# Kernel optimization log

Measured on AMD Instinct MI355X. Metric: run time of the kernel, lower is better.

Reference implementation:

```python
import jax, jax.numpy as jnp
import numpy as np

N = 500_000
E = 5_000_000
DIM = 16
LR = 0.005
THRESHOLD = 0.0


def setup_inputs() -> dict:
    key = jax.random.key(0)
    ks = jax.random.split(key, 8)
    s = 1.0 / np.sqrt(DIM)
    return {
        "x": jax.random.normal(ks[0], (N, DIM), jnp.float32),
        "edge_index": jax.random.randint(ks[1], (2, E), 0, N, dtype=jnp.int32),
        "W1": jax.random.normal(ks[2], (DIM, DIM), jnp.float32) * s,
        "b1": jnp.zeros((DIM,), jnp.float32),
        "W2": jax.random.normal(ks[3], (DIM, DIM), jnp.float32) * s,
        "b2": jnp.zeros((DIM,), jnp.float32),
        "W3": jax.random.normal(ks[4], (DIM, DIM), jnp.float32) * s,
        "b3": jnp.zeros((DIM,), jnp.float32),
        "positive": 0,  # negative sample -> nonzero loss branch
    }


def gcn_conv(x, edge_index, W, b):
    # PyG GCNConv: h = x @ W.T, add self-loops, symmetric norm, aggregate at dst.
    n = x.shape[0]
    loop = jnp.arange(n, dtype=edge_index.dtype)
    src = jnp.concatenate([edge_index[0], loop])
    dst = jnp.concatenate([edge_index[1], loop])
    deg = jax.ops.segment_sum(jnp.ones_like(dst, x.dtype), dst, num_segments=n)
    dinv = jnp.where(deg > 0, jax.lax.rsqrt(deg), 0.0)
    norm = dinv[src] * dinv[dst]  # [E+N]
    h = x @ W.T  # [N, out]
    msg = norm[:, None] * h[src]  # irregular gather, memory-bound
    return jax.ops.segment_sum(msg, dst, num_segments=n) + b


def local_loss(g, positive):
    t = THRESHOLD
    if positive:
        return jnp.where(g > t + 10.0, 0.0,
               jnp.where(g < t - 10.0, t - g, jnp.log1p(jnp.exp(t - g))))
    return jnp.where(g > t + 10.0, t + g,
           jnp.where(g < t - 10.0, 0.0, jnp.log1p(jnp.exp(g + t))))


def reference(x, edge_index, W1, b1, W2, b2, W3, b3, positive):
    # Note: the original computes activation_normalizer(x) and loss_derivative(g)
    # into z/driv_loss but immediately overwrites both -> dead code, omitted.
    agg = jnp.float32(0.0)
    Wc, bc = W1, b1  # conv1 params, updated in-place each layer in the original
    x_cur = x
    for (W, b) in ((W1, b1), (W2, b2), (W3, b3)):
        z = jax.nn.relu(gcn_conv(x_cur, edge_index, W, b))
        goodness = jnp.sum(z * z) / z.shape[1]
        agg = agg + local_loss(goodness, positive)
        d = 2.0 * jnp.abs(z)            # activation_gradient(z)
        wd = d * d                      # weighted_deriv
        dW = x_cur.T @ wd               # [in, out]
        db = jnp.sum(wd, axis=0)
        Wc = Wc - LR * dW.T
        bc = bc - LR * db
        x_cur = z
    return agg, Wc, bc
```

## Files before the change

kernel.cpp:

```cpp
#include <hip/hip_runtime.h>
#include <math.h>

#define TPB 256
#define TPB_P 512
#define TPB_A 512
#define LRATE 0.005f

#define LOG_NPB 10
#define NPB (1 << LOG_NPB)
#define CAP 14336

#define LOG_SUP 13
#define NS1 64
#define CAP1 90112
#define NS2 8
#define CHUNK 4096
#define CPT (CHUNK / TPB_P)
#define R1 4
#define R2 8
#define RS 4

#define NTILE 64

#define FXS  65536.0f
#define FXSI (1.0f / 65536.0f)
#define FXBIAS (1 << 20)

#if __has_builtin(__builtin_amdgcn_cvt_f32_fp8) && __has_builtin(__builtin_amdgcn_cvt_pk_fp8_f32)
__device__ __forceinline__ float fp8_dec(unsigned char v) {
    return __builtin_amdgcn_cvt_f32_fp8((int)v, 0);
}
__device__ __forceinline__ unsigned fp8_pk4(float a, float b, float c, float d) {
    int w = __builtin_amdgcn_cvt_pk_fp8_f32(a, b, 0, false);
    w = __builtin_amdgcn_cvt_pk_fp8_f32(c, d, w, true);
    return (unsigned)w;
}
#else
__device__ __forceinline__ unsigned char fp8_enc1(float f) {
    unsigned u = __float_as_uint(f);
    unsigned s = (u >> 24) & 0x80u;
    u &= 0x7FFFFFFFu;
    if (u >= 0x43E00000u) return (unsigned char)(s | 0x7E);
    if (u < 0x3C800000u) {
        float a = __uint_as_float(u);
        int m = (int)rintf(a * 512.f);
        return (unsigned char)(s | (unsigned)m);
    }
    unsigned mant = u & 0x7FFFFFu;
    unsigned rest = mant & 0xFFFFFu;
    unsigned keep = u >> 20;
    keep += (rest > 0x80000u || (rest == 0x80000u && (keep & 1u))) ? 1u : 0u;
    int eb = (int)(keep >> 3) - 127 + 7;
    return (unsigned char)(s | (unsigned)((eb << 3) | (int)(keep & 7u)));
}
__device__ __forceinline__ float fp8_dec(unsigned char v) {
    unsigned s = ((unsigned)(v & 0x80u)) << 24;
    unsigned e = (v >> 3) & 0xFu;
    unsigned m = v & 7u;
    if (e == 0) {
        float r = (float)m * 0.001953125f;
        return (v & 0x80u) ? -r : r;
    }
    return __uint_as_float(s | ((e + 120u) << 23) | (m << 20));
}
__device__ __forceinline__ unsigned fp8_pk4(float a, float b, float c, float d) {
    return (unsigned)fp8_enc1(a) | ((unsigned)fp8_enc1(b) << 8) |
           ((unsigned)fp8_enc1(c) << 16) | ((unsigned)fp8_enc1(d) << 24);
}
#endif

#if __has_builtin(__builtin_amdgcn_cvt_pk_f32_fp8)
typedef float __attribute__((ext_vector_type(2))) f32x2;
__device__ __forceinline__ void fp8_dec4(unsigned w, float& a, float& b, float& c, float& d) {
    f32x2 lo = __builtin_amdgcn_cvt_pk_f32_fp8((int)w, false);
    f32x2 hi = __builtin_amdgcn_cvt_pk_f32_fp8((int)w, true);
    a = lo[0]; b = lo[1]; c = hi[0]; d = hi[1];
}
#else
__device__ __forceinline__ void fp8_dec4(unsigned w, float& a, float& b, float& c, float& d) {
    a = fp8_dec((unsigned char)(w & 0xFFu));
    b = fp8_dec((unsigned char)((w >> 8) & 0xFFu));
    c = fp8_dec((unsigned char)((w >> 16) & 0xFFu));
    d = fp8_dec((unsigned char)((w >> 24) & 0xFFu));
}
#endif

__device__ __forceinline__ unsigned long long pack2(float f0, float f1) {
    unsigned lo = (unsigned)(FXBIAS + (int)(f0 * FXS));
    unsigned hi = (unsigned)(FXBIAS + (int)(f1 * FXS));
    return (unsigned long long)lo | ((unsigned long long)hi << 32);
}

__global__ __launch_bounds__(TPB_P) void k_part1(const int* __restrict__ src,
                                                 const int* __restrict__ dst,
                                                 int* __restrict__ bcur1,
                                                 int* __restrict__ grec1,
                                                 int E) {
    __shared__ int hist[R1][NS1];
    __shared__ int lcur[R1][NS1];
    __shared__ int lstart[NS1], tot[NS1], gbase[NS1];
    __shared__ int lbuf[CHUNK];
    __shared__ unsigned char bbuf[CHUNK];
    int t = threadIdx.x;
    int g = t & (R1 - 1);
    int chunkBase = blockIdx.x * CHUNK;
    for (int i = t; i < R1 * NS1; i += TPB_P) (&hist[0][0])[i] = 0;
    __syncthreads();

    int myb[CPT], myrec[CPT];
#pragma unroll
    for (int k = 0; k < CPT; k++) {
        int e = chunkBase + k * TPB_P + t;
        if (e < E) {
            int d = dst[e];
            int s = src[e];
            myb[k] = d >> LOG_SUP;
            myrec[k] = (s << LOG_SUP) | (d & ((1 << LOG_SUP) - 1));
            atomicAdd(&hist[g][myb[k]], 1);
        } else myb[k] = -1;
    }
    __syncthreads();
    if (t < NS1) {
        int s = 0;
#pragma unroll
        for (int r = 0; r < R1; r++) s += hist[r][t];
        tot[t] = s;
    }
    __syncthreads();
    if (t == 0) {
        int run = 0;
        for (int b = 0; b < NS1; b++) { lstart[b] = run; run += tot[b]; }
    }
    __syncthreads();
    if (t < NS1) {
        int run = lstart[t];
#pragma unroll
        for (int r = 0; r < R1; r++) { lcur[r][t] = run; run += hist[r][t]; }
        if (tot[t] > 0) gbase[t] = atomicAdd(&bcur1[t * 16], tot[t]);
    }
    __syncthreads();
#pragma unroll
    for (int k = 0; k < CPT; k++) {
        if (myb[k] >= 0) {
            int p = atomicAdd(&lcur[g][myb[k]], 1);
            lbuf[p] = myrec[k];
            bbuf[p] = (unsigned char)myb[k];
        }
    }
    __syncthreads();
    int total = E - chunkBase; if (total > CHUNK) total = CHUNK;
    for (int p = t; p < total; p += TPB_P) {
        int b = (int)bbuf[p];
        int pos = gbase[b] + (p - lstart[b]);
        if (pos < CAP1) grec1[(size_t)b * CAP1 + pos] = lbuf[p];
    }
}

__global__ __launch_bounds__(TPB_P) void k_part2(const int* __restrict__ bcur1,
                                                 const int* __restrict__ grec1,
                                                 int* __restrict__ bcur,
                                                 int* __restrict__ grecU) {
    __shared__ int hist[R2][NS2];
    __shared__ int lcur[R2][NS2];
    __shared__ int lstart[NS2], tot[NS2], gbase[NS2];
    __shared__ int lbuf[CHUNK];
    __shared__ unsigned char bbuf[CHUNK];
    int t = threadIdx.x;
    int g = t & (R2 - 1);
    int s = blockIdx.x;
    int cnt1 = bcur1[s * 16]; if (cnt1 > CAP1) cnt1 = CAP1;
    int chunkBase = blockIdx.y * CHUNK;
    if (chunkBase >= cnt1) return;
    int total = cnt1 - chunkBase; if (total > CHUNK) total = CHUNK;
    for (int i = t; i < R2 * NS2; i += TPB_P) (&hist[0][0])[i] = 0;
    __syncthreads();

    int myb[CPT], myrec[CPT];
#pragma unroll
    for (int k = 0; k < CPT; k++) {
        int i = chunkBase + k * TPB_P + t;
        if (i < cnt1) {
            int r = grec1[(size_t)s * CAP1 + i];
            int sub = (r >> LOG_NPB) & (NS2 - 1);
            myb[k] = sub;
            myrec[k] = (int)((((unsigned)r) >> LOG_SUP) << LOG_NPB) | (r & (NPB - 1));
            atomicAdd(&hist[g][sub], 1);
        } else myb[k] = -1;
    }
    __syncthreads();
    if (t < NS2) {
        int c = 0;
#pragma unroll
        for (int r = 0; r < R2; r++) c += hist[r][t];
        tot[t] = c;
    }
    __syncthreads();
    if (t == 0) {
        int run = 0;
        for (int b = 0; b < NS2; b++) { lstart[b] = run; run += tot[b]; }
    }
    __syncthreads();
    if (t < NS2) {
        int run = lstart[t];
#pragma unroll
        for (int r = 0; r < R2; r++) { lcur[r][t] = run; run += hist[r][t]; }
        if (tot[t] > 0) gbase[t] = atomicAdd(&bcur[(s * NS2 + t) * 16], tot[t]);
    }
    __syncthreads();
#pragma unroll
    for (int k = 0; k < CPT; k++) {
        if (myb[k] >= 0) {
            int p = atomicAdd(&lcur[g][myb[k]], 1);
            lbuf[p] = myrec[k];
            bbuf[p] = (unsigned char)myb[k];
        }
    }
    __syncthreads();
    for (int p = t; p < total; p += TPB_P) {
        int b = (int)bbuf[p];
        int pos = gbase[b] + (p - lstart[b]);
        if (pos < CAP) grecU[(size_t)(s * NS2 + b) * CAP + pos] = lbuf[p];
    }
}

__global__ __launch_bounds__(TPB_P) void k_sort(const int* __restrict__ bcur,
                                                const int* __restrict__ grecU,
                                                int* __restrict__ grec,
                                                float* __restrict__ dinv, int N) {
    __shared__ int lbuf[CAP];
    __shared__ int deg[NPB];
    __shared__ int hist[RS][NTILE];
    __shared__ int curp[RS][NTILE];
    __shared__ int lstart[NTILE], tot[NTILE];
    int t = threadIdx.x;
    int g = t & (RS - 1);
    int b = blockIdx.x;
    int cnt = bcur[b * 16]; if (cnt > CAP) cnt = CAP;
    const size_t base = (size_t)b * CAP;

    for (int i = t; i < RS * NTILE; i += TPB_P) (&hist[0][0])[i] = 0;
    for (int i = t; i < NPB; i += TPB_P) deg[i] = 0;
    __syncthreads();
    for (int i = t; i < cnt; i += TPB_P) {
        int r = grecU[base + i];
        lbuf[i] = r;
        atomicAdd(&deg[r & (NPB - 1)], 1);
        atomicAdd(&hist[g][((unsigned)r) >> 23], 1);
    }
    __syncthreads();
    if (t < NTILE) {
        int c = 0;
#pragma unroll
        for (int r = 0; r < RS; r++) c += hist[r][t];
        tot[t] = c;
    }
    __syncthreads();
    if (t == 0) {
        int run = 0;
#pragma unroll
        for (int k = 0; k < NTILE; k++) { lstart[k] = run; run += tot[k]; }
    }
    __syncthreads();
    if (t < NTILE) {
        int run = lstart[t];
#pragma unroll
        for (int r = 0; r < RS; r++) { curp[r][t] = run; run += hist[r][t]; }
    }
    __syncthreads();
    for (int i = t; i < cnt; i += TPB_P) {
        int r = lbuf[i];
        int p = atomicAdd(&curp[g][((unsigned)r) >> 23], 1);
        grec[base + p] = r;
    }
    int nodeBase = b << LOG_NPB;
    for (int i = t; i < NPB; i += TPB_P) {
        int node = nodeBase + i;
        if (node < N) dinv[node] = rsqrtf((float)(deg[i] + 1));
    }
}

__global__ __launch_bounds__(TPB) void k_h(const float* __restrict__ xc,
                                           const float* __restrict__ W,
                                           const float* __restrict__ dinv,
                                           unsigned* __restrict__ hp, int n) {
    __shared__ float sW[256];
    if (threadIdx.x < 256) sW[threadIdx.x] = W[threadIdx.x];
    __syncthreads();
    int i = blockIdx.x * blockDim.x + threadIdx.x;
    int stride = gridDim.x * blockDim.x;
    for (; i < n; i += stride) {
        float x[16];
        const float4* xr = (const float4*)(xc + (size_t)i * 16);
#pragma unroll
        for (int q = 0; q < 4; q++) {
            float4 v = xr[q];
            x[4*q+0] = v.x; x[4*q+1] = v.y; x[4*q+2] = v.z; x[4*q+3] = v.w;
        }
        float di = dinv[i];
        float hv[16];
#pragma unroll
        for (int j = 0; j < 16; j++) {
            float s = 0.f;
#pragma unroll
            for (int k = 0; k < 16; k++) s = fmaf(x[k], sW[j*16 + k], s);
            hv[j] = di * s;
        }
        uint4 w;
        w.x = fp8_pk4(hv[0],  hv[1],  hv[2],  hv[3]);
        w.y = fp8_pk4(hv[4],  hv[5],  hv[6],  hv[7]);
        w.z = fp8_pk4(hv[8],  hv[9],  hv[10], hv[11]);
        w.w = fp8_pk4(hv[12], hv[13], hv[14], hv[15]);
        ((uint4*)hp)[i] = w;
    }
}

__global__ __launch_bounds__(TPB_A, 4) void k_agg(const int* __restrict__ bcur,
                                                  const int* __restrict__ grec,
                                                  const float* __restrict__ dinv,
                                                  const unsigned* __restrict__ hp32,
                                                  const float* __restrict__ b,
                                                  const float* __restrict__ xc,
                                                  float* __restrict__ z,
                                                  float* __restrict__ partial,
                                                  int nb, int N) {
    __shared__ unsigned long long accP[8 * NPB];
    int t = threadIdx.x;
    int bkt = blockIdx.x;
    int cnt = bcur[bkt * 16]; if (cnt > CAP) cnt = CAP;
    const int nodeBase = bkt << LOG_NPB;
    const size_t recBase = (size_t)bkt * CAP;

    for (int i = t; i < 8 * NPB; i += TPB_A) accP[i] = 0ull;
    __syncthreads();

    int q = t & 3;
    int gi = t >> 2;
    int p0 = q * 2;
    int p1 = q * 2 + 1;
    int base = 0;
    for (; base + 512 <= cnt; base += 512) {
        int rec[4];
#pragma unroll
        for (int u = 0; u < 4; u++) rec[u] = grec[recBase + base + u * 128 + gi];
        unsigned w[4];
#pragma unroll
        for (int u = 0; u < 4; u++)
            w[u] = hp32[(size_t)(((unsigned)rec[u]) >> LOG_NPB) * 4 + q];
#pragma unroll
        for (int u = 0; u < 4; u++) {
            int dl = rec[u] & (NPB - 1);
            float f0, f1, f2, f3;
            fp8_dec4(w[u], f0, f1, f2, f3);
            atomicAdd(&accP[p0 * NPB + (dl ^ p0)], pack2(f0, f1));
            atomicAdd(&accP[p1 * NPB + (dl ^ p1)], pack2(f2, f3));
        }
    }
    for (int e = base + gi; e < cnt; e += 128) {
        int rec = grec[recBase + e];
        unsigned w = hp32[(size_t)(((unsigned)rec) >> LOG_NPB) * 4 + q];
        int dl = rec & (NPB - 1);
        float f0, f1, f2, f3;
        fp8_dec4(w, f0, f1, f2, f3);
        atomicAdd(&accP[p0 * NPB + (dl ^ p0)], pack2(f0, f1));
        atomicAdd(&accP[p1 * NPB + (dl ^ p1)], pack2(f2, f3));
    }
    __syncthreads();

    const unsigned char* hpB = (const unsigned char*)hp32;
    const int* accI32 = (const int*)accP;
    int j = t & 15;
    int g0 = t >> 4;
    int pj = j >> 1;
    int hj = j & 1;
    float bj = b[j];
    float accW[16];
#pragma unroll
    for (int k = 0; k < 16; k++) accW[k] = 0.f;
    float accB = 0.f;

    for (int i = g0; i < NPB; i += 32) {
        int node = nodeBase + i;
        if (node >= N) break;
        float di = dinv[node];
        int cdeg = (int)rintf(1.0f / (di * di)) - 1;
        int raw = accI32[(pj * NPB + (i ^ pj)) * 2 + hj];
        int ai = raw - cdeg * FXBIAS;
        float sv = fp8_dec(hpB[(size_t)node * 16 + j]);
        float aj = fmaf((float)ai, FXSI, sv);
        float zj = fmaxf(fmaf(di, aj, bj), 0.f);
        z[(size_t)node * 16 + j] = zj;
        float wdj = 4.f * zj * zj;
        accB += wdj;
        const float4* xrow = (const float4*)(xc + (size_t)node * 16);
        float4 x0 = xrow[0], x1 = xrow[1], x2 = xrow[2], x3 = xrow[3];
        accW[0]  = fmaf(x0.x, wdj, accW[0]);  accW[1]  = fmaf(x0.y, wdj, accW[1]);
        accW[2]  = fmaf(x0.z, wdj, accW[2]);  accW[3]  = fmaf(x0.w, wdj, accW[3]);
        accW[4]  = fmaf(x1.x, wdj, accW[4]);  accW[5]  = fmaf(x1.y, wdj, accW[5]);
        accW[6]  = fmaf(x1.z, wdj, accW[6]);  accW[7]  = fmaf(x1.w, wdj, accW[7]);
        accW[8]  = fmaf(x2.x, wdj, accW[8]);  accW[9]  = fmaf(x2.y, wdj, accW[9]);
        accW[10] = fmaf(x2.z, wdj, accW[10]); accW[11] = fmaf(x2.w, wdj, accW[11]);
        accW[12] = fmaf(x3.x, wdj, accW[12]); accW[13] = fmaf(x3.y, wdj, accW[13]);
        accW[14] = fmaf(x3.z, wdj, accW[14]); accW[15] = fmaf(x3.w, wdj, accW[15]);
    }
    __syncthreads();

    float (*red)[17] = (float (*)[17])accP;
#pragma unroll
    for (int k = 0; k < 16; k++) red[t][k] = accW[k];
    red[t][16] = accB;
    __syncthreads();
    if (t < 256) {
        int kk = t >> 4;
        int jj = t & 15;
        float s = 0.f;
#pragma unroll
        for (int g2 = 0; g2 < 32; g2++) s += red[g2 * 16 + jj][kk];
        partial[(size_t)(kk * 16 + jj) * nb + bkt] = s;
    }
    if (t < 16) {
        float sb = 0.f;
#pragma unroll
        for (int g2 = 0; g2 < 32; g2++) sb += red[g2 * 16 + t][16];
        partial[(size_t)(256 + t) * nb + bkt] = sb;
    }
}

__global__ __launch_bounds__(TPB) void k_reduce(const float* __restrict__ partial,
                                                float* __restrict__ acc,
                                                int nb, int total) {
    int wid = (blockIdx.x * blockDim.x + threadIdx.x) >> 6;
    int lane = threadIdx.x & 63;
    if (wid >= total) return;
    const float* p = partial + (size_t)wid * nb;
    float s = 0.f;
    for (int b = lane; b < nb; b += 64) s += p[b];
#pragma unroll
    for (int off = 32; off > 0; off >>= 1) s += __shfl_down(s, off, 64);
    if (lane == 0) acc[wid] = s;
}

__device__ __forceinline__ float local_loss_f(float g, int positive) {
    const float t = 0.0f;
    if (positive) {
        if (g > t + 10.f) return 0.f;
        if (g < t - 10.f) return t - g;
        return log1pf(expf(t - g));
    } else {
        if (g > t + 10.f) return t + g;
        if (g < t - 10.f) return 0.f;
        return log1pf(expf(g + t));
    }
}

__global__ void k_final(const float* __restrict__ W1, const float* __restrict__ b1,
                        const float* __restrict__ acc, const int* __restrict__ positive,
                        float* __restrict__ outv) {
    int t = threadIdx.x;
    if (t < 256) {
        int jj = t >> 4, kk = t & 15;
        float s = 0.f;
#pragma unroll
        for (int l = 0; l < 3; l++) s += acc[l * 272 + kk * 16 + jj];
        outv[1 + t] = W1[t] - LRATE * s;
    }
    if (t < 16) {
        float s = 0.f;
#pragma unroll
        for (int l = 0; l < 3; l++) s += acc[l * 272 + 256 + t];
        outv[257 + t] = b1[t] - LRATE * s;
    }
    if (t == 0) {
        int pos = positive[0];
        float agg = 0.f;
#pragma unroll
        for (int l = 0; l < 3; l++) {
            float g = 0.f;
#pragma unroll
            for (int jj = 0; jj < 16; jj++) g += acc[l * 272 + 256 + jj];
            g *= (1.0f / 64.0f);
            agg += local_loss_f(g, pos);
        }
        outv[0] = agg;
    }
}

extern "C" void kernel_launch(void* const* d_in, const int* in_sizes, int n_in,
                              void* d_out, int out_size, void* d_ws, size_t ws_size,
                              hipStream_t stream) {
    const float* x  = (const float*)d_in[0];
    const int*   ei = (const int*)d_in[1];
    const float* W1 = (const float*)d_in[2];
    const float* b1 = (const float*)d_in[3];
    const float* W2 = (const float*)d_in[4];
    const float* b2 = (const float*)d_in[5];
    const float* W3 = (const float*)d_in[6];
    const float* b3 = (const float*)d_in[7];
    const int* positive = (const int*)d_in[8];
    float* outv = (float*)d_out;

    const int N = in_sizes[0] / 16;
    const int E = in_sizes[1] / 2;
    const int nbuck = (N + NPB - 1) >> LOG_NPB;
    const int nsuper = (N + (1 << LOG_SUP) - 1) >> LOG_SUP;
    const int nbpad = nsuper * NS2;

    char* ws = (char*)d_ws;
    size_t off = 0;
    auto carve = [&](size_t bytes) -> void* {
        void* p = ws + off;
        off = (off + bytes + 255) & ~(size_t)255;
        return p;
    };
    int*   bcur   = (int*)  carve((size_t)(nbpad + NS1) * 16 * 4);
    int*   bcur1  = bcur + (size_t)nbpad * 16;
    int*   grec   = (int*)  carve((size_t)nbpad * CAP * 4);
    float* dinv   = (float*)carve((size_t)N * 4);
    float* acc    = (float*)carve(3 * 272 * 4);
    float* part   = (float*)carve((size_t)3 * 272 * nbuck * 4);
    unsigned* hp  = (unsigned*)carve((size_t)N * 16);
    float* P1     = (float*)carve((size_t)N * 64);
    int*   grecU  = (int*)P1;
    float* P2     = (float*)carve((size_t)N * 64);
    int*   grec1  = (int*)P2;

    hipMemsetAsync(bcur, 0, (size_t)(nbpad + NS1) * 16 * 4, stream);

    const int* src = ei;
    const int* dst = ei + E;

    int p1Blocks = (E + CHUNK - 1) / CHUNK;
    k_part1<<<p1Blocks, TPB_P, 0, stream>>>(src, dst, bcur1, grec1, E);
    dim3 g2(nsuper, CAP1 / CHUNK);
    k_part2<<<g2, TPB_P, 0, stream>>>(bcur1, grec1, bcur, grecU);
    k_sort<<<nbuck, TPB_P, 0, stream>>>(bcur, grecU, grec, dinv, N);

    const float* Ws[3] = {W1, W2, W3};
    const float* bss[3] = {b1, b2, b3};
    float* outs[3] = {P1, P2, P1};

    int nodeBlocks = (N + TPB - 1) / TPB;

    const float* xc = x;
    for (int l = 0; l < 3; l++) {
        k_h<<<nodeBlocks, TPB, 0, stream>>>(xc, Ws[l], dinv, hp, N);
        k_agg<<<nbuck, TPB_A, 0, stream>>>(bcur, grec, dinv, hp, bss[l],
                                           xc, outs[l],
                                           part + (size_t)l * 272 * nbuck, nbuck, N);
        xc = outs[l];
    }
    int totalElems = 3 * 272;
    k_reduce<<<(totalElems * 64 + TPB - 1) / TPB, TPB, 0, stream>>>(part, acc, nbuck, totalElems);
    k_final<<<1, 256, 0, stream>>>(W1, b1, acc, positive, outv);
}
```

Before: 391.4 us.

## Fuse per-layer h projection into sort and aggregation kernel epilogues

Removes the separate k_h launches. The first layer's fp8 h = dinv*(x@W1^T) is now computed at the end of k_sort. Each later layer's h is computed in the epilogue of the previous k_agg, reading the z rows that block just wrote, with the hp buffer double-buffered between layers. This saves three kernel launches and lets z be reread while it is likely still cache-resident. In exchange the aggregation kernels get longer tails with extra syncs and register pressure inside a kernel bound to 4 waves per SIMD.

After: 657.2 us. 1.68x slower.

```diff
diff --git a/kernel.cpp b/kernel.cpp
--- a/kernel.cpp
+++ b/kernel.cpp
@@ -19,7 +19,6 @@
 #define R1 4
 #define R2 8
 #define RS 4
-
 #define NTILE 64
 
 #define FXS  65536.0f
@@ -89,6 +88,31 @@
     unsigned lo = (unsigned)(FXBIAS + (int)(f0 * FXS));
     unsigned hi = (unsigned)(FXBIAS + (int)(f1 * FXS));
     return (unsigned long long)lo | ((unsigned long long)hi << 32);
+}
+
+__device__ __forceinline__ uint4 hp_row(const float* __restrict__ xrow,
+                                        const float* __restrict__ sW, float di) {
+    float xv[16];
+    const float4* xr = (const float4*)xrow;
+#pragma unroll
+    for (int q = 0; q < 4; q++) {
+        float4 v = xr[q];
+        xv[4*q+0] = v.x; xv[4*q+1] = v.y; xv[4*q+2] = v.z; xv[4*q+3] = v.w;
+    }
+    float hv[16];
+#pragma unroll
+    for (int j = 0; j < 16; j++) {
+        float s = 0.f;
+#pragma unroll
+        for (int k = 0; k < 16; k++) s = fmaf(xv[k], sW[j*16 + k], s);
+        hv[j] = di * s;
+    }
+    uint4 w;
+    w.x = fp8_pk4(hv[0],  hv[1],  hv[2],  hv[3]);
+    w.y = fp8_pk4(hv[4],  hv[5],  hv[6],  hv[7]);
+    w.z = fp8_pk4(hv[8],  hv[9],  hv[10], hv[11]);
+    w.w = fp8_pk4(hv[12], hv[13], hv[14], hv[15]);
+    return w;
 }
 
 __global__ __launch_bounds__(TPB_P) void k_part1(const int* __restrict__ src,
@@ -226,7 +250,10 @@
 __global__ __launch_bounds__(TPB_P) void k_sort(const int* __restrict__ bcur,
                                                 const int* __restrict__ grecU,
                                                 int* __restrict__ grec,
-                                                float* __restrict__ dinv, int N) {
+                                                float* __restrict__ dinv,
+                                                const float* __restrict__ x,
+                                                const float* __restrict__ W1,
+                                                unsigned* __restrict__ hp, int N) {
     __shared__ int lbuf[CAP];
     __shared__ int deg[NPB];
     __shared__ int hist[RS][NTILE];
@@ -272,45 +299,18 @@
         int p = atomicAdd(&curp[g][((unsigned)r) >> 23], 1);
         grec[base + p] = r;
     }
+    __syncthreads();
+
+    float* sW = (float*)lbuf;
+    if (t < 256) sW[t] = W1[t];
+    __syncthreads();
     int nodeBase = b << LOG_NPB;
     for (int i = t; i < NPB; i += TPB_P) {
         int node = nodeBase + i;
-        if (node < N) dinv[node] = rsqrtf((float)(deg[i] + 1));
-    }
-}
-
-__global__ __launch_bounds__(TPB) void k_h(const float* __restrict__ xc,
-                                           const float* __restrict__ W,
-                                           const float* __restrict__ dinv,
-                                           unsigned* __restrict__ hp, int n) {
-    __shared__ float sW[256];
-    if (threadIdx.x < 256) sW[threadIdx.x] = W[threadIdx.x];
-    __syncthreads();
-    int i = blockIdx.x * blockDim.x + threadIdx.x;
-    int stride = gridDim.x * blockDim.x;
-    for (; i < n; i += stride) {
-        float x[16];
-        const float4* xr = (const float4*)(xc + (size_t)i * 16);
-#pragma unroll
-        for (int q = 0; q < 4; q++) {
-            float4 v = xr[q];
-            x[4*q+0] = v.x; x[4*q+1] = v.y; x[4*q+2] = v.z; x[4*q+3] = v.w;
-        }
-        float di = dinv[i];
-        float hv[16];
-#pragma unroll
-        for (int j = 0; j < 16; j++) {
-            float s = 0.f;
-#pragma unroll
-            for (int k = 0; k < 16; k++) s = fmaf(x[k], sW[j*16 + k], s);
-            hv[j] = di * s;
-        }
-        uint4 w;
-        w.x = fp8_pk4(hv[0],  hv[1],  hv[2],  hv[3]);
-        w.y = fp8_pk4(hv[4],  hv[5],  hv[6],  hv[7]);
-        w.z = fp8_pk4(hv[8],  hv[9],  hv[10], hv[11]);
-        w.w = fp8_pk4(hv[12], hv[13], hv[14], hv[15]);
-        ((uint4*)hp)[i] = w;
+        if (node >= N) continue;
+        float di = rsqrtf((float)(deg[i] + 1));
+        dinv[node] = di;
+        ((uint4*)hp)[node] = hp_row(x + (size_t)node * 16, sW, di);
     }
 }
 
@@ -322,6 +322,8 @@
                                                   const float* __restrict__ xc,
                                                   float* __restrict__ z,
                                                   float* __restrict__ partial,
+                                                  const float* __restrict__ Wnext,
+                                                  unsigned* __restrict__ hpNext,
                                                   int nb, int N) {
     __shared__ unsigned long long accP[8 * NPB];
     int t = threadIdx.x;
@@ -423,6 +425,18 @@
         for (int g2 = 0; g2 < 32; g2++) sb += red[g2 * 16 + t][16];
         partial[(size_t)(256 + t) * nb + bkt] = sb;
     }
+
+    if (Wnext != nullptr) {
+        __syncthreads();
+        float* sW = (float*)accP;
+        if (t < 256) sW[t] = Wnext[t];
+        __syncthreads();
+        for (int i = t; i < NPB; i += TPB_A) {
+            int node = nodeBase + i;
+            if (node >= N) continue;
+            ((uint4*)hpNext)[node] = hp_row(z + (size_t)node * 16, sW, dinv[node]);
+        }
+    }
 }
 
 __global__ __launch_bounds__(TPB) void k_reduce(const float* __restrict__ partial,
@@ -517,7 +531,8 @@
     float* dinv   = (float*)carve((size_t)N * 4);
     float* acc    = (float*)carve(3 * 272 * 4);
     float* part   = (float*)carve((size_t)3 * 272 * nbuck * 4);
-    unsigned* hp  = (unsigned*)carve((size_t)N * 16);
+    unsigned* hpA = (unsigned*)carve((size_t)N * 16);
+    unsigned* hpB = (unsigned*)carve((size_t)N * 16);
     float* P1     = (float*)carve((size_t)N * 64);
     int*   grecU  = (int*)P1;
     float* P2     = (float*)carve((size_t)N * 64);
@@ -532,22 +547,18 @@
     k_part1<<<p1Blocks, TPB_P, 0, stream>>>(src, dst, bcur1, grec1, E);
     dim3 g2(nsuper, CAP1 / CHUNK);
     k_part2<<<g2, TPB_P, 0, stream>>>(bcur1, grec1, bcur, grecU);
-    k_sort<<<nbuck, TPB_P, 0, stream>>>(bcur, grecU, grec, dinv, N);
-
-    const float* Ws[3] = {W1, W2, W3};
-    const float* bss[3] = {b1, b2, b3};
-    float* outs[3] = {P1, P2, P1};
-
-    int nodeBlocks = (N + TPB - 1) / TPB;
-
-    const float* xc = x;
-    for (int l = 0; l < 3; l++) {
-        k_h<<<nodeBlocks, TPB, 0, stream>>>(xc, Ws[l], dinv, hp, N);
-        k_agg<<<nbuck, TPB_A, 0, stream>>>(bcur, grec, dinv, hp, bss[l],
-                                           xc, outs[l],
-                                           part + (size_t)l * 272 * nbuck, nbuck, N);
-        xc = outs[l];
-    }
+    k_sort<<<nbuck, TPB_P, 0, stream>>>(bcur, grecU, grec, dinv, x, W1, hpA, N);
+
+    k_agg<<<nbuck, TPB_A, 0, stream>>>(bcur, grec, dinv, hpA, b1, x,  P1,
+                                       part + (size_t)0 * 272 * nbuck,
+                                       W2, hpB, nbuck, N);
+    k_agg<<<nbuck, TPB_A, 0, stream>>>(bcur, grec, dinv, hpB, b2, P1, P2,
+                                       part + (size_t)1 * 272 * nbuck,
+                                       W3, hpA, nbuck, N);
+    k_agg<<<nbuck, TPB_A, 0, stream>>>(bcur, grec, dinv, hpA, b3, P2, P1,
+                                       part + (size_t)2 * 272 * nbuck,
+                                       nullptr, nullptr, nbuck, N);
+
     int totalElems = 3 * 272;
     k_reduce<<<(totalElems * 64 + TPB - 1) / TPB, TPB, 0, stream>>>(part, acc, nbuck, totalElems);
     k_final<<<1, 256, 0, stream>>>(W1, b1, acc, positive, outv);
```
